# Performance work log

Hardware: AMD Instinct MI355X
Metric: run time of the kernel (lower is better)

The kernel has to match this reference:

```python
import jax, jax.numpy as jnp
import numpy as np

B, N, C, H, K = 16, 1024, 384, 6, 8
HID = int(C * 2.0)  # mlp_ratio = 2.0
HD = C // H


def _layernorm(x, w, b, eps=1e-5):
    m = x.mean(-1, keepdims=True)
    v = ((x - m) ** 2).mean(-1, keepdims=True)
    return (x - m) * jax.lax.rsqrt(v + eps) * w + b


def setup_inputs() -> dict:
    key = jax.random.key(0)
    ks = jax.random.split(key, 16)
    x = jax.random.normal(ks[0], (B, N, C), jnp.float32)
    # knn indices within each batch, offset by batch*N (as in get_knn_index)
    idx = jax.random.randint(ks[1], (B, K, N), 0, N)
    base = jnp.arange(B, dtype=jnp.int32)[:, None, None] * N
    knn_index = (idx + base).reshape(-1).astype(jnp.int32)
    s = 0.02
    p = {
        "x": x,
        "knn_index": knn_index,
        "ln1_w": jnp.ones((C,), jnp.float32),
        "ln1_b": jnp.zeros((C,), jnp.float32),
        "w_qkv": jax.random.normal(ks[2], (C, 3 * C), jnp.float32) * s,  # qkv_bias=False
        "w_proj": jax.random.normal(ks[3], (C, C), jnp.float32) * s,
        "b_proj": jnp.zeros((C,), jnp.float32),
        "w_knn": jax.random.normal(ks[4], (2 * C, C), jnp.float32) * s,
        "b_knn": jnp.zeros((C,), jnp.float32),
        "w_merge": jax.random.normal(ks[5], (2 * C, C), jnp.float32) * s,
        "b_merge": jnp.zeros((C,), jnp.float32),
        "ln2_w": jnp.ones((C,), jnp.float32),
        "ln2_b": jnp.zeros((C,), jnp.float32),
        "w_fc1": jax.random.normal(ks[6], (C, HID), jnp.float32) * s,
        "b_fc1": jnp.zeros((HID,), jnp.float32),
        "w_fc2": jax.random.normal(ks[7], (HID, C), jnp.float32) * s,
        "b_fc2": jnp.zeros((C,), jnp.float32),
    }
    return p


def reference(x, knn_index, ln1_w, ln1_b, w_qkv, w_proj, b_proj, w_knn, b_knn,
              w_merge, b_merge, ln2_w, ln2_b, w_fc1, b_fc1, w_fc2, b_fc2):
    nx = _layernorm(x, ln1_w, ln1_b)  # [B,N,C]

    # --- self attention ---
    qkv = (nx @ w_qkv).reshape(B, N, 3, H, HD)
    q, k, v = qkv[:, :, 0], qkv[:, :, 1], qkv[:, :, 2]  # [B,N,H,HD]
    scale = HD ** (-0.5)
    attn = jnp.einsum("bnhd,bmhd->bhnm", q, k) * scale
    attn = jax.nn.softmax(attn, axis=-1)
    a_out = jnp.einsum("bhnm,bmhd->bnhd", attn, v).reshape(B, N, C)
    x1 = a_out @ w_proj + b_proj

    # --- graph feature: gather, relative concat, Linear+LeakyReLU, max over k ---
    feat = nx.reshape(B * N, C)[knn_index].reshape(B, K, N, C)
    center = nx[:, None, :, :]  # [B,1,N,C]
    g = jnp.concatenate([feat - center, jnp.broadcast_to(center, (B, K, N, C))], axis=-1)
    knn_f = jax.nn.leaky_relu(g @ w_knn + b_knn, negative_slope=0.2)
    knn_f = knn_f.max(axis=1)  # [B,N,C]

    x1 = jnp.concatenate([x1, knn_f], axis=-1) @ w_merge + b_merge
    x = x + x1

    # --- MLP ---
    h = _layernorm(x, ln2_w, ln2_b)
    h = jax.nn.gelu(h @ w_fc1 + b_fc1, approximate=False) @ w_fc2 + b_fc2
    return x + h
```

## Files before the change

kernel.cpp:

```cpp
#include <hip/hip_runtime.h>
#include <hip/hip_bf16.h>
#include <math.h>

#define BN_ROWS 16384
#define CDIM 384
#define NH 6
#define BBATCH 16
#define NNN 1024

typedef unsigned short u16;
typedef unsigned int u32;
typedef __attribute__((ext_vector_type(8))) short short8;
typedef __attribute__((ext_vector_type(4))) float floatx4;

__device__ __forceinline__ float b2f(u16 s) { return __uint_as_float(((u32)s) << 16); }
__device__ __forceinline__ u16 f2b(float f) {
    __hip_bfloat16 h = __float2bfloat16(f);
    u16 s; __builtin_memcpy(&s, &h, 2); return s;
}
__device__ __forceinline__ u32 cvt_pk_bf16(float lo, float hi) {
    u32 r;
    asm("v_cvt_pk_bf16_f32 %0, %1, %2" : "=v"(r) : "v"(lo), "v"(hi));
    return r;
}
__device__ __forceinline__ void gload_lds16(const u16* g, u16* l) {
    __builtin_amdgcn_global_load_lds(
        (const __attribute__((address_space(1))) unsigned int*)g,
        (__attribute__((address_space(3))) unsigned int*)l, 16, 0, 0);
}

__global__ __launch_bounds__(256) void pack_all(
    const float* __restrict__ W0, u16* __restrict__ T0,
    const float* __restrict__ W1, u16* __restrict__ T1,
    const float* __restrict__ W2, u16* __restrict__ T2,
    const float* __restrict__ W3, u16* __restrict__ T3,
    const float* __restrict__ W4, u16* __restrict__ T4,
    const float* __restrict__ W5, u16* __restrict__ T5)
{
    const float* W; u16* T; int K, N;
    switch (blockIdx.z) {
        case 0: W = W0; T = T0; K = 384; N = 1152; break;
        case 1: W = W1; T = T1; K = 384; N = 384;  break;
        case 2: W = W2; T = T2; K = 768; N = 384;  break;
        case 3: W = W3; T = T3; K = 768; N = 384;  break;
        case 4: W = W4; T = T4; K = 384; N = 768;  break;
        default: W = W5; T = T5; K = 768; N = 384; break;
    }
    const int n0 = blockIdx.x * 32, k0 = blockIdx.y * 32;
    if (n0 >= N || k0 >= K) return;
    __shared__ float s[32][33];
    const int tx = threadIdx.x & 31, ty = threadIdx.x >> 5;
#pragma unroll
    for (int i = 0; i < 4; ++i)
        s[ty + 8 * i][tx] = W[(size_t)(k0 + ty + 8 * i) * N + n0 + tx];
    __syncthreads();
#pragma unroll
    for (int i = 0; i < 4; ++i)
        T[(size_t)(n0 + ty + 8 * i) * K + k0 + tx] = f2b(s[tx][ty + 8 * i]);
}

__global__ __launch_bounds__(64) void ln_kernel(const float* __restrict__ xin,
                                                const float* __restrict__ w,
                                                const float* __restrict__ b,
                                                u16* __restrict__ out)
{
    const int row = blockIdx.x;
    const int t = threadIdx.x;
    const size_t base = (size_t)row * CDIM;
    float v[6];
#pragma unroll
    for (int i = 0; i < 6; ++i) v[i] = xin[base + t + 64 * i];
    float s = 0.f, s2 = 0.f;
#pragma unroll
    for (int i = 0; i < 6; ++i) { s += v[i]; s2 += v[i] * v[i]; }
#pragma unroll
    for (int m = 1; m < 64; m <<= 1) {
        s  += __shfl_xor(s,  m, 64);
        s2 += __shfl_xor(s2, m, 64);
    }
    const float mean = s * (1.0f / CDIM);
    const float var  = s2 * (1.0f / CDIM) - mean * mean;
    const float rs   = rsqrtf(var + 1e-5f);
#pragma unroll
    for (int i = 0; i < 6; ++i) {
        int c = t + 64 * i;
        out[base + c] = f2b((v[i] - mean) * rs * w[c] + b[c]);
    }
}

template<int ACT, bool HAS_BIAS, bool HAS_RES, bool OUT_F32, int MODE, int NT, bool SWZ>
__global__ __launch_bounds__(256) void gemm_mfma_kernel(
    const u16* __restrict__ A, int lda,
    const u16* __restrict__ Bt, const u16* __restrict__ Bt2, int ldbt,
    u16* Cb, u16* Cb2, float* Cf, int ldc,
    const float* __restrict__ bias,
    const float* res,
    int K)
{
    constexpr int NTL = NT / 32;
    __shared__ u16 As[2][128 * 32];
    __shared__ u16 Bs[2][NT * 32];
    const int tid  = threadIdx.x;
    const int wv   = tid >> 6;
    const int lane = tid & 63;
    const int l15  = lane & 15;
    const int quad = lane >> 4;

    int m0, n0;
    if (SWZ) {
        const int nbx = gridDim.x;
        const int total = nbx * gridDim.y;
        int lin = blockIdx.x + nbx * blockIdx.y;
        const int cpx = total >> 3;
        lin = (lin & 7) * cpx + (lin >> 3);
        m0 = (lin / nbx) * 128;
        n0 = (lin % nbx) * NT;
    } else {
        m0 = blockIdx.y * 128;
        n0 = blockIdx.x * NT;
    }

    const int woffm = (wv >> 1) * 64;
    const int woffn = (wv & 1) * (NT / 2);

    const u16* bsrc = (MODE == 2 && n0 >= 384) ? Bt2 : Bt;
    const int  bn0  = (MODE == 2 && n0 >= 384) ? (n0 - 384) : n0;

    floatx4 acc[4][NTL];
#pragma unroll
    for (int mt = 0; mt < 4; ++mt)
#pragma unroll
        for (int nt = 0; nt < NTL; ++nt) acc[mt][nt] = (floatx4){0.f, 0.f, 0.f, 0.f};

    const int gsw  = 8 * ((lane & 3) ^ ((lane >> 3) & 3));
    const int rloc = lane >> 2;
    const int rdsw = 8 * (quad ^ ((l15 >> 1) & 3));

    auto stage = [&](int kt, int p) {
#pragma unroll
        for (int j = 0; j < 2; ++j) {
            const int slab = 32 * wv + 16 * j;
            gload_lds16(A + (size_t)(m0 + slab + rloc) * lda + kt + gsw, &As[p][slab * 32]);
        }
        if (NT == 128) {
#pragma unroll
            for (int j = 0; j < 2; ++j) {
                const int slab = 32 * wv + 16 * j;
                gload_lds16(bsrc + (size_t)(bn0 + slab + rloc) * ldbt + kt + gsw, &Bs[p][slab * 32]);
            }
        } else {
            const int slab = 16 * wv;
            gload_lds16(bsrc + (size_t)(bn0 + slab + rloc) * ldbt + kt + gsw, &Bs[p][slab * 32]);
        }
    };

    stage(0, 0);
    __syncthreads();
    int cur = 0;
    for (int kt = 0; kt < K; kt += 32) {
        if (kt + 32 < K) stage(kt + 32, cur ^ 1);

        short8 af[4], bf[NTL];
#pragma unroll
        for (int mt = 0; mt < 4; ++mt)
            af[mt] = *(const short8*)(As[cur] + (woffm + mt * 16 + l15) * 32 + rdsw);
#pragma unroll
        for (int nt = 0; nt < NTL; ++nt)
            bf[nt] = *(const short8*)(Bs[cur] + (woffn + nt * 16 + l15) * 32 + rdsw);
#pragma unroll
        for (int mt = 0; mt < 4; ++mt)
#pragma unroll
            for (int nt = 0; nt < NTL; ++nt)
                acc[mt][nt] = __builtin_amdgcn_mfma_f32_16x16x32_bf16(
                    bf[nt], af[mt], acc[mt][nt], 0, 0, 0);
        __syncthreads();
        cur ^= 1;
    }

#pragma unroll
    for (int mt = 0; mt < 4; ++mt) {
        const int gr = m0 + woffm + mt * 16 + l15;
#pragma unroll
        for (int nt = 0; nt < NTL; ++nt) {
            const int gc0 = n0 + woffn + nt * 16 + quad * 4;
            float v4[4];
#pragma unroll
            for (int rr = 0; rr < 4; ++rr) v4[rr] = acc[mt][nt][rr];
            if (HAS_BIAS) {
                const floatx4 bv = *(const floatx4*)(bias + gc0);
#pragma unroll
                for (int rr = 0; rr < 4; ++rr) v4[rr] += bv[rr];
            }
            if (MODE == 2) {
                if (gc0 >= 384) {
                    const floatx4 bv = *(const floatx4*)(bias + gc0 - 384);
#pragma unroll
                    for (int rr = 0; rr < 4; ++rr) v4[rr] += bv[rr];
                }
            }
            if (ACT == 1) {
#pragma unroll
                for (int rr = 0; rr < 4; ++rr)
                    v4[rr] = 0.5f * v4[rr] * (1.0f + erff(v4[rr] * 0.70710678118654752f));
            }
            if (HAS_RES) {
                const floatx4 rv = *(const floatx4*)(res + (size_t)gr * ldc + gc0);
#pragma unroll
                for (int rr = 0; rr < 4; ++rr) v4[rr] += rv[rr];
            }
            if (MODE == 1) {
                const int t3  = gc0 / 384;
                const int rem = gc0 - t3 * 384;
                const int hh = rem >> 6, dd = rem & 63;
                const int bb = gr >> 10, nn = gr & 1023;
                u32 lo = cvt_pk_bf16(v4[0], v4[1]);
                u32 hi = cvt_pk_bf16(v4[2], v4[3]);
                *(uint2*)(Cb + ((size_t)((bb * 6 + hh) * 1024 + nn)) * 192 + t3 * 64 + dd) =
                    make_uint2(lo, hi);
            } else if (MODE == 2) {
                u32 lo = cvt_pk_bf16(v4[0], v4[1]);
                u32 hi = cvt_pk_bf16(v4[2], v4[3]);
                if (gc0 < 384)
                    *(uint2*)(Cb  + (size_t)gr * 384 + gc0)       = make_uint2(lo, hi);
                else
                    *(uint2*)(Cb2 + (size_t)gr * 384 + gc0 - 384) = make_uint2(lo, hi);
            } else if (OUT_F32) {
                floatx4 vv = {v4[0], v4[1], v4[2], v4[3]};
                *(floatx4*)(Cf + (size_t)gr * ldc + gc0) = vv;
            } else {
                u32 lo = cvt_pk_bf16(v4[0], v4[1]);
                u32 hi = cvt_pk_bf16(v4[2], v4[3]);
                *(uint2*)(Cb + (size_t)gr * ldc + gc0) = make_uint2(lo, hi);
            }
        }
    }
}

__global__ __launch_bounds__(256) void attn_mfma_kernel(const u16* __restrict__ qkv2,
                                                        u16* __restrict__ aout)
{
    const int id = blockIdx.x;
    const int rxcd = id & 7;
    const int j = id >> 3;
    const int slab = rxcd + 8 * (j % 12);
    const int qtile = j / 12;
    const int b = slab / NH, h = slab % NH;

    const int wave = threadIdx.x >> 6;
    const int lane = threadIdx.x & 63;
    const int l15 = lane & 15;
    const int quad = lane >> 4;
    const int qbase = qtile * 128 + wave * 32;
    const int tid = threadIdx.x;

    const u16* slabp = qkv2 + ((size_t)(b * NH + h) << 10) * 192;

    __shared__ __align__(16) u16 Ks[64 * 72];
    __shared__ __align__(16) u16 Vt[64 * 72];
    __shared__ __align__(16) u16 Ps[4][32 * 72];
    __shared__ __align__(16) float Ls[4][32];

    short8 qf[2][2];
#pragma unroll
    for (int nt = 0; nt < 2; ++nt) {
        const u16* qrow = slabp + (size_t)(qbase + nt * 16 + l15) * 192;
        qf[nt][0] = *(const short8*)(qrow + quad * 8);
        qf[nt][1] = *(const short8*)(qrow + 32 + quad * 8);
    }

    float rowsum[2] = {0.f, 0.f};
    floatx4 Oacc[2][4];
#pragma unroll
    for (int mt = 0; mt < 2; ++mt)
#pragma unroll
        for (int nt = 0; nt < 4; ++nt) Oacc[mt][nt] = (floatx4){0.f, 0.f, 0.f, 0.f};

    for (int kc = 0; kc < NNN; kc += 64) {
        {
            const int key = tid >> 2, dblk = (tid & 3) * 16;
            const u16* kp = slabp + (size_t)(kc + key) * 192 + 64 + dblk;
            *(short8*)(Ks + key * 72 + dblk)     = *(const short8*)(kp);
            *(short8*)(Ks + key * 72 + dblk + 8) = *(const short8*)(kp + 8);
        }
        {
            const int kp2 = tid & 31, db = (tid >> 5) * 8;
            const u16* v0p = slabp + (size_t)(kc + 2 * kp2) * 192 + 128 + db;
            uint4 v0 = *(const uint4*)(v0p);
            uint4 v1 = *(const uint4*)(v0p + 192);
            u32 a0[4] = {v0.x, v0.y, v0.z, v0.w};
            u32 a1[4] = {v1.x, v1.y, v1.z, v1.w};
#pragma unroll
            for (int i = 0; i < 4; ++i) {
                u32 lo = __builtin_amdgcn_perm(a1[i], a0[i], 0x05040100u);
                u32 hi = __builtin_amdgcn_perm(a1[i], a0[i], 0x07060302u);
                *(u32*)(Vt + (size_t)(db + 2 * i)     * 72 + 2 * kp2) = lo;
                *(u32*)(Vt + (size_t)(db + 2 * i + 1) * 72 + 2 * kp2) = hi;
            }
        }
        __syncthreads();

        floatx4 sc[4][2];
        __builtin_amdgcn_s_setprio(1);
#pragma unroll
        for (int kt_ = 0; kt_ < 4; ++kt_) {
            short8 kf0 = *(const short8*)(Ks + (kt_ * 16 + l15) * 72 + quad * 8);
            short8 kf1 = *(const short8*)(Ks + (kt_ * 16 + l15) * 72 + 32 + quad * 8);
#pragma unroll
            for (int nt = 0; nt < 2; ++nt) {
                floatx4 s = {0.f, 0.f, 0.f, 0.f};
                s = __builtin_amdgcn_mfma_f32_16x16x32_bf16(kf0, qf[nt][0], s, 0, 0, 0);
                s = __builtin_amdgcn_mfma_f32_16x16x32_bf16(kf1, qf[nt][1], s, 0, 0, 0);
                sc[kt_][nt] = s;
            }
        }
        __builtin_amdgcn_s_setprio(0);

#pragma unroll
        for (int kt_ = 0; kt_ < 4; ++kt_)
#pragma unroll
            for (int nt = 0; nt < 2; ++nt) {
                float pv[4];
#pragma unroll
                for (int rr = 0; rr < 4; ++rr) {
                    pv[rr] = __expf(sc[kt_][nt][rr] * 0.125f);
                    rowsum[nt] += pv[rr];
                }
                u32 lo = cvt_pk_bf16(pv[0], pv[1]);
                u32 hi = cvt_pk_bf16(pv[2], pv[3]);
                *(uint2*)(Ps[wave] + (nt * 16 + l15) * 72 + kt_ * 16 + quad * 4) =
                    make_uint2(lo, hi);
            }

        short8 pf[2][2];
#pragma unroll
        for (int mt = 0; mt < 2; ++mt) {
            pf[mt][0] = *(const short8*)(Ps[wave] + (mt * 16 + l15) * 72 + quad * 8);
            pf[mt][1] = *(const short8*)(Ps[wave] + (mt * 16 + l15) * 72 + 32 + quad * 8);
        }
        __builtin_amdgcn_s_setprio(1);
#pragma unroll
        for (int nt = 0; nt < 4; ++nt) {
#pragma unroll
            for (int kk = 0; kk < 2; ++kk) {
                short8 vf = *(const short8*)(Vt + (size_t)(nt * 16 + l15) * 72 + kk * 32 + quad * 8);
#pragma unroll
                for (int mt = 0; mt < 2; ++mt)
                    Oacc[mt][nt] = __builtin_amdgcn_mfma_f32_16x16x32_bf16(
                        pf[mt][kk], vf, Oacc[mt][nt], 0, 0, 0);
            }
        }
        __builtin_amdgcn_s_setprio(0);
        __syncthreads();
    }

#pragma unroll
    for (int nt = 0; nt < 2; ++nt) {
        float l = rowsum[nt];
        l += __shfl_xor(l, 16, 64);
        l += __shfl_xor(l, 32, 64);
        if (quad == 0) Ls[wave][nt * 16 + l15] = l;
    }
#pragma unroll
    for (int mt = 0; mt < 2; ++mt) {
        float4 lv = *(const float4*)&Ls[wave][mt * 16 + quad * 4];
        float li[4] = {lv.x, lv.y, lv.z, lv.w};
#pragma unroll
        for (int rr = 0; rr < 4; ++rr) {
            float inv = 1.0f / li[rr];
            int q = qbase + mt * 16 + quad * 4 + rr;
#pragma unroll
            for (int nt = 0; nt < 4; ++nt)
                aout[(size_t)(b * NNN + q) * CDIM + h * 64 + nt * 16 + l15] =
                    f2b(Oacc[mt][nt][rr] * inv);
        }
    }
}

__global__ __launch_bounds__(128) void knnmax_kernel(const u16* __restrict__ t1,
                                                     const u16* __restrict__ t2,
                                                     const int* __restrict__ idx,
                                                     u16* __restrict__ x1cat)
{
    const int bn = blockIdx.x * 2 + (threadIdx.x >> 6);
    const int lane = threadIdx.x & 63;
    if (lane >= 48) return;
    const int b = bn >> 10, n = bn & 1023;
    int ind[8];
#pragma unroll
    for (int k = 0; k < 8; ++k) ind[k] = idx[b * 8192 + k * 1024 + n];
    const int c0 = lane * 8;
    const size_t rbase = (size_t)bn * CDIM + c0;
    short8 v1 = *(const short8*)(t1 + rbase);
    short8 v2 = *(const short8*)(t2 + rbase);
    float basef[8], mx[8];
#pragma unroll
    for (int j = 0; j < 8; ++j) {
        basef[j] = b2f((u16)v2[j]) - b2f((u16)v1[j]);
        mx[j] = -1e30f;
    }
#pragma unroll
    for (int k = 0; k < 8; ++k) {
        short8 nv = *(const short8*)(t1 + (size_t)ind[k] * CDIM + c0);
#pragma unroll
        for (int j = 0; j < 8; ++j) {
            float v = b2f((u16)nv[j]) + basef[j];
            v = (v > 0.f) ? v : 0.2f * v;
            mx[j] = fmaxf(mx[j], v);
        }
    }
    short8 ov;
#pragma unroll
    for (int j = 0; j < 8; ++j) ov[j] = (short)f2b(mx[j]);
    *(short8*)(x1cat + (size_t)bn * 768 + CDIM + c0) = ov;
}

extern "C" void kernel_launch(void* const* d_in, const int* in_sizes, int n_in,
                              void* d_out, int out_size, void* d_ws, size_t ws_size,
                              hipStream_t stream)
{
    (void)in_sizes; (void)n_in; (void)out_size; (void)ws_size;
    const float* x     = (const float*)d_in[0];
    const int*   knn   = (const int*)d_in[1];
    const float* ln1w  = (const float*)d_in[2];
    const float* ln1b  = (const float*)d_in[3];
    const float* wqkv  = (const float*)d_in[4];
    const float* wproj = (const float*)d_in[5];
    const float* bproj = (const float*)d_in[6];
    const float* wknn  = (const float*)d_in[7];
    const float* bknn  = (const float*)d_in[8];
    const float* wmrg  = (const float*)d_in[9];
    const float* bmrg  = (const float*)d_in[10];
    const float* ln2w  = (const float*)d_in[11];
    const float* ln2b  = (const float*)d_in[12];
    const float* wfc1  = (const float*)d_in[13];
    const float* bfc1  = (const float*)d_in[14];
    const float* wfc2  = (const float*)d_in[15];
    const float* bfc2  = (const float*)d_in[16];

    u16* wsb = (u16*)d_ws;
    const size_t RE = (size_t)BN_ROWS * CDIM;
    u16* nxb   = wsb;
    u16* qkvb  = wsb + RE;
    u16* x1cat = wsb + RE;
    u16* t1b   = wsb + 3 * RE;
    u16* hinb  = wsb;
    u16* h1b   = wsb + RE;
    u16* wqkvT  = wsb + 4 * RE;
    u16* wprojT = wqkvT + 442368;
    u16* wknnT  = wprojT + 147456;
    u16* wmrgT  = wknnT + 294912;
    u16* wfc1T  = wmrgT + 294912;
    u16* wfc2T  = wfc1T + 294912;
    u16*   aoutb = (u16*)d_out;
    u16*   t2b   = (u16*)d_out;
    float* xmid  = (float*)d_out;

    pack_all<<<dim3(36, 24, 6), 256, 0, stream>>>(
        wqkv, wqkvT, wproj, wprojT, wknn, wknnT, wmrg, wmrgT, wfc1, wfc1T, wfc2, wfc2T);
    ln_kernel<<<BN_ROWS, 64, 0, stream>>>(x, ln1w, ln1b, nxb);
    gemm_mfma_kernel<0, false, false, false, 1, 128, true><<<dim3(9, 128), 256, 0, stream>>>(
        nxb, CDIM, wqkvT, nullptr, CDIM, qkvb, nullptr, nullptr, 0, nullptr, nullptr, CDIM);
    attn_mfma_kernel<<<768, 256, 0, stream>>>(qkvb, aoutb);
    gemm_mfma_kernel<0, true, false, false, 0, 64, true><<<dim3(6, 128), 256, 0, stream>>>(
        aoutb, CDIM, wprojT, nullptr, CDIM, x1cat, nullptr, nullptr, 768, bproj, nullptr, CDIM);
    gemm_mfma_kernel<0, false, false, false, 2, 128, true><<<dim3(6, 128), 256, 0, stream>>>(
        nxb, CDIM, wknnT, wknnT + 384, 768, t1b, t2b, nullptr, CDIM, bknn, nullptr, CDIM);
    knnmax_kernel<<<BN_ROWS / 2, 128, 0, stream>>>(t1b, t2b, knn, x1cat);
    gemm_mfma_kernel<0, true, true, true, 0, 64, true><<<dim3(6, 128), 256, 0, stream>>>(
        x1cat, 768, wmrgT, nullptr, 768, nullptr, nullptr, xmid, CDIM, bmrg, x, 768);
    ln_kernel<<<BN_ROWS, 64, 0, stream>>>(xmid, ln2w, ln2b, hinb);
    gemm_mfma_kernel<1, true, false, false, 0, 128, true><<<dim3(6, 128), 256, 0, stream>>>(
        hinb, CDIM, wfc1T, nullptr, CDIM, h1b, nullptr, nullptr, 768, bfc1, nullptr, CDIM);
    gemm_mfma_kernel<0, true, true, true, 0, 64, true><<<dim3(6, 128), 256, 0, stream>>>(
        h1b, 768, wfc2T, nullptr, 768, nullptr, nullptr, (float*)d_out, CDIM, bfc2, xmid, 768);
}
```

Baseline: 312.4 us.

## Deepen GEMM LDS prefetch pipeline and register-prefetch K/V tiles in attention

The GEMM main loop now keeps two stages of async global-to-LDS loads in flight. It waits with explicit vmcnt counts and raw s_barrier instead of a full __syncthreads, and issues the stage for kt+64 after the MFMA block. The attention kernel loads the next K/V chunk into registers while the current chunk is being computed, then writes it to LDS at the top of the next iteration. Both changes aim to hide global-memory latency behind MFMA work. The cost is extra VGPR pressure and fragile hand-tuned vmcnt values that must match the number of loads issued per stage.

Result: no change. 309.2 us (-1.0%).

```diff
diff --git a/kernel.cpp b/kernel.cpp
--- a/kernel.cpp
+++ b/kernel.cpp
@@ -155,10 +155,18 @@
     };
 
     stage(0, 0);
-    __syncthreads();
+    stage(32, 1);
     int cur = 0;
     for (int kt = 0; kt < K; kt += 32) {
-        if (kt + 32 < K) stage(kt + 32, cur ^ 1);
+        if (kt + 32 < K) {
+            if constexpr (NT == 128) asm volatile("s_waitcnt vmcnt(4)" ::: "memory");
+            else                     asm volatile("s_waitcnt vmcnt(3)" ::: "memory");
+        } else {
+            asm volatile("s_waitcnt vmcnt(0)" ::: "memory");
+        }
+        __builtin_amdgcn_sched_barrier(0);
+        __builtin_amdgcn_s_barrier();
+        __builtin_amdgcn_sched_barrier(0);
 
         short8 af[4], bf[NTL];
 #pragma unroll
@@ -173,7 +181,10 @@
             for (int nt = 0; nt < NTL; ++nt)
                 acc[mt][nt] = __builtin_amdgcn_mfma_f32_16x16x32_bf16(
                     bf[nt], af[mt], acc[mt][nt], 0, 0, 0);
-        __syncthreads();
+        __builtin_amdgcn_sched_barrier(0);
+        __builtin_amdgcn_s_barrier();
+        __builtin_amdgcn_sched_barrier(0);
+        if (kt + 64 < K) stage(kt + 64, cur);
         cur ^= 1;
     }
 
@@ -275,20 +286,24 @@
 #pragma unroll
         for (int nt = 0; nt < 4; ++nt) Oacc[mt][nt] = (floatx4){0.f, 0.f, 0.f, 0.f};
 
+    const int key = tid >> 2, dblk = (tid & 3) * 16;
+    const int kp2 = tid & 31, db = (tid >> 5) * 8;
+    uint4 kr0, kr1, vr0, vr1;
+    {
+        const u16* kp = slabp + (size_t)key * 192 + 64 + dblk;
+        kr0 = *(const uint4*)(kp);
+        kr1 = *(const uint4*)(kp + 8);
+        const u16* vp = slabp + (size_t)(2 * kp2) * 192 + 128 + db;
+        vr0 = *(const uint4*)(vp);
+        vr1 = *(const uint4*)(vp + 192);
+    }
+
     for (int kc = 0; kc < NNN; kc += 64) {
+        *(uint4*)(Ks + key * 72 + dblk)     = kr0;
+        *(uint4*)(Ks + key * 72 + dblk + 8) = kr1;
         {
-            const int key = tid >> 2, dblk = (tid & 3) * 16;
-            const u16* kp = slabp + (size_t)(kc + key) * 192 + 64 + dblk;
-            *(short8*)(Ks + key * 72 + dblk)     = *(const short8*)(kp);
-            *(short8*)(Ks + key * 72 + dblk + 8) = *(const short8*)(kp + 8);
-        }
-        {
-            const int kp2 = tid & 31, db = (tid >> 5) * 8;
-            const u16* v0p = slabp + (size_t)(kc + 2 * kp2) * 192 + 128 + db;
-            uint4 v0 = *(const uint4*)(v0p);
-            uint4 v1 = *(const uint4*)(v0p + 192);
-            u32 a0[4] = {v0.x, v0.y, v0.z, v0.w};
-            u32 a1[4] = {v1.x, v1.y, v1.z, v1.w};
+            u32 a0[4] = {vr0.x, vr0.y, vr0.z, vr0.w};
+            u32 a1[4] = {vr1.x, vr1.y, vr1.z, vr1.w};
 #pragma unroll
             for (int i = 0; i < 4; ++i) {
                 u32 lo = __builtin_amdgcn_perm(a1[i], a0[i], 0x05040100u);
@@ -298,6 +313,15 @@
             }
         }
         __syncthreads();
+
+        if (kc + 64 < NNN) {
+            const u16* kp = slabp + (size_t)(kc + 64 + key) * 192 + 64 + dblk;
+            kr0 = *(const uint4*)(kp);
+            kr1 = *(const uint4*)(kp + 8);
+            const u16* vp = slabp + (size_t)(kc + 64 + 2 * kp2) * 192 + 128 + db;
+            vr0 = *(const uint4*)(vp);
+            vr1 = *(const uint4*)(vp + 192);
+        }
 
         floatx4 sc[4][2];
         __builtin_amdgcn_s_setprio(1);
```
